# Optimization experiments

Hardware: AMD Instinct MI355X
Metric: run time of the kernel (lower is better)

The kernel has to match this reference:

```python
import jax, jax.numpy as jnp
import numpy as np

B, C, H, W = 64, 3, 32, 32
HID, PRE, VMAX = 128, 32, 256
IN_DIM = C * 5 - 1  # 14


def setup_inputs() -> dict:
    key = jax.random.key(0)
    ks = jax.random.split(key, 9)
    s = 0.05
    return {
        "x": jax.random.uniform(ks[0], (B, C, H, W), dtype=jnp.float32),
        "W_pre": jax.random.normal(ks[1], (PRE, IN_DIM), dtype=jnp.float32) * s,
        "b_pre": jnp.zeros((PRE,), dtype=jnp.float32),
        "W_ih": jax.random.normal(ks[2], (3 * HID, PRE), dtype=jnp.float32) * s,
        "b_ih": jnp.zeros((3 * HID,), dtype=jnp.float32),
        "W_hh": jax.random.normal(ks[3], (3 * HID, HID), dtype=jnp.float32) * s,
        "b_hh": jnp.zeros((3 * HID,), dtype=jnp.float32),
        "W_post": jax.random.normal(ks[4], (VMAX, HID), dtype=jnp.float32) * s,
        "b_post": jnp.zeros((VMAX,), dtype=jnp.float32),
    }


def _img2input(x):
    # x: [b, c, h, w] -> [b, (h-2)*(w-2)*c, 5c-1], matching torch _img2input
    b, c, h, w = x.shape
    xp = jnp.transpose(x, (0, 2, 3, 1))  # [b,h,w,c]
    tl = xp[:, :-2, :-2, :]
    tc = xp[:, :-2, 1:-1, :]
    tr = xp[:, :-2, 2:, :]
    lf = xp[:, 1:-1, :-2, :]
    ct = xp[:, 1:-1, 1:-1, :]
    base = jnp.concatenate([tl, tc, tr, lf], axis=-1)  # [b,h-2,w-2,4c]
    base = jnp.broadcast_to(base[..., None, :], base.shape[:3] + (c, 4 * c))
    # tail[ic, ic1] = center[ic1] if ic1 < ic else -1
    mask = jnp.arange(c - 1)[None, :] < jnp.arange(c)[:, None]  # [c, c-1]
    tail = jnp.where(mask, ct[..., None, :c - 1], -1.0)  # [b,h-2,w-2,c,c-1]
    y = jnp.concatenate([base, tail], axis=-1)  # [b,h-2,w-2,c,5c-1]
    return y.reshape(b, (h - 2) * (w - 2) * c, 5 * c - 1)


def reference(x, W_pre, b_pre, W_ih, b_ih, W_hh, b_hh, W_post, b_post):
    b, c, h, w = x.shape
    inp = _img2input(x)                                   # [b, T, 5c-1]
    pre = jax.nn.sigmoid(inp @ W_pre.T + b_pre)           # [b, T, PRE]
    xg = pre @ W_ih.T + b_ih                              # [b, T, 3*HID]
    xg_t = jnp.transpose(xg, (1, 0, 2))                   # [T, b, 3*HID]

    def step(h_prev, xt):
        hg = h_prev @ W_hh.T + b_hh
        xr, xz, xn = jnp.split(xt, 3, axis=-1)
        hr, hz, hn = jnp.split(hg, 3, axis=-1)
        r = jax.nn.sigmoid(xr + hr)
        z = jax.nn.sigmoid(xz + hz)
        n = jnp.tanh(xn + r * hn)
        h_new = (1.0 - z) * n + z * h_prev
        return h_new, h_new

    h0 = jnp.zeros((b, W_hh.shape[1]), dtype=x.dtype)
    _, hs = jax.lax.scan(step, h0, xg_t)                  # [T, b, HID]
    hs = jnp.transpose(hs, (1, 0, 2))                     # [b, T, HID]
    out = hs @ W_post.T + b_post                          # [b, T, VMAX]
    vmax = W_post.shape[0]
    out = out.reshape(b, h - 2, w - 2, c, vmax)
    out = jnp.transpose(out, (0, 3, 1, 2, 4))             # [b, c, h-2, w-2, vmax]
    out = jnp.pad(out, ((0, 0), (0, 0), (1, 1), (1, 1), (0, 0)))
    return out  # [b, c, h, w, vmax]
```

## Files before the change

### kernel.cpp

```cpp
#include <hip/hip_runtime.h>
#include <cstdint>

#define B_    64
#define T_    2700
#define HID_  128
#define PRE_  32
#define VMAX_ 256
#define NG_   16
#define NB_   4
#define TCH_  27
#define TSZ_  100

typedef _Float16 half2_t __attribute__((ext_vector_type(2)));
typedef _Float16 half4_t __attribute__((ext_vector_type(4)));
typedef _Float16 half8_t __attribute__((ext_vector_type(8)));
typedef float    f32x4_t __attribute__((ext_vector_type(4)));
union H8u { half8_t v; half2_t p[4]; };

#define MFMA32(A, Bv, C) __builtin_amdgcn_mfma_f32_16x16x32_f16((A), (Bv), (C), 0, 0, 0)

#if __has_builtin(__builtin_amdgcn_fdot2)
__device__ __forceinline__ float FDOT2(half2_t a, half2_t b, float c) {
    return __builtin_amdgcn_fdot2(a, b, c, false);
}
#else
__device__ __forceinline__ float FDOT2(half2_t a, half2_t b, float c) {
    return c + (float)a[0] * (float)b[0] + (float)a[1] * (float)b[1];
}
#endif

__device__ __forceinline__ half2_t mk2(float a, float b) {
    half2_t r; r[0] = (_Float16)a; r[1] = (_Float16)b; return r;
}
__device__ __forceinline__ float fast_sigmoid(float x) {
    float t = __builtin_amdgcn_exp2f(-1.4426950408889634f * x);
    return __builtin_amdgcn_rcpf(1.0f + t);
}
__device__ __forceinline__ float fast_tanh(float x) {
    float t = __builtin_amdgcn_exp2f(2.885390081777927f * x);
    return 1.0f - 2.0f * __builtin_amdgcn_rcpf(t + 1.0f);
}
__device__ __forceinline__ float pick_reg(f32x4_t v, int addr, int sel) {
    float t0 = __int_as_float(__builtin_amdgcn_ds_bpermute(addr, __float_as_int(v[0])));
    float t1 = __int_as_float(__builtin_amdgcn_ds_bpermute(addr, __float_as_int(v[1])));
    float t2 = __int_as_float(__builtin_amdgcn_ds_bpermute(addr, __float_as_int(v[2])));
    float t3 = __int_as_float(__builtin_amdgcn_ds_bpermute(addr, __float_as_int(v[3])));
    float a = (sel & 1) ? t1 : t0;
    float b = (sel & 1) ? t3 : t2;
    return (sel & 2) ? b : a;
}

__global__ __launch_bounds__(256) void k_pre(const float* __restrict__ x,
                                             const float* __restrict__ W_pre,
                                             const float* __restrict__ b_pre,
                                             _Float16* __restrict__ pre16) {
    int tid  = blockIdx.x * 256 + threadIdx.x;
    int i    = tid & 31;
    int rest = tid >> 5;
    int c    = rest % 3;
    int r2   = rest / 3;
    int p    = r2 % 900;
    int b    = r2 / 900;
    int r    = p / 30;
    int cc   = p - r * 30;
    const float* xb = x + b * 3072 + r * 32 + cc;
    float f0 = xb[0],    f1  = xb[1024], f2  = xb[2048];
    float f3 = xb[1],    f4  = xb[1025], f5  = xb[2049];
    float f6 = xb[2],    f7  = xb[1026], f8  = xb[2050];
    float f9 = xb[32],   f10 = xb[1056], f11 = xb[2080];
    float ct0 = xb[33],  ct1 = xb[1057];
    float f12 = (c >= 1) ? ct0 : -1.0f;
    float f13 = (c >= 2) ? ct1 : -1.0f;
    const float* w = W_pre + i * 14;
    float d = b_pre[i];
    d += f0*w[0]  + f1*w[1]  + f2*w[2]  + f3*w[3]  + f4*w[4]  + f5*w[5]  + f6*w[6]
       + f7*w[7]  + f8*w[8]  + f9*w[9]  + f10*w[10] + f11*w[11] + f12*w[12] + f13*w[13];

    int t  = p * 3 + c;
    int g  = b >> 2;
    int cs = b & 3;
    size_t base = ((size_t)g * T_ + t) * 128;
    int idx = ((i >> 3) << 5) | (cs << 3) | (i & 7);
    pre16[base + idx] = (_Float16)fast_sigmoid(d);
}

__global__ __launch_bounds__(512) void k_xg(const float* __restrict__ W_ih,
                                            const float* __restrict__ b_ih,
                                            const float* __restrict__ b_hh,
                                            const _Float16* __restrict__ pre16,
                                            _Float16* __restrict__ xg16) {
    const int tid = threadIdx.x;
    const int g   = blockIdx.x / TCH_;
    const int tc  = blockIdx.x % TCH_;
    const int u3  = (tid >> 6) * 16 + ((tid & 63) >> 2);
    const int c4  = tid & 3;

    half2_t wr[16], wz[16], wn[16];
    const float* Wr = W_ih + (size_t)u3 * PRE_;
    const float* Wz = W_ih + (size_t)(128 + u3) * PRE_;
    const float* Wn = W_ih + (size_t)(256 + u3) * PRE_;
#pragma unroll
    for (int k2 = 0; k2 < 16; ++k2) {
        wr[k2] = mk2(Wr[2*k2], Wr[2*k2 + 1]);
        wz[k2] = mk2(Wz[2*k2], Wz[2*k2 + 1]);
        wn[k2] = mk2(Wn[2*k2], Wn[2*k2 + 1]);
    }
    const float br = b_ih[u3] + b_hh[u3];
    const float bz = b_ih[128 + u3] + b_hh[128 + u3];
    const float bn = b_ih[256 + u3];

    const char* preg = (const char*)pre16 + ((size_t)g * T_ + (size_t)tc * TSZ_) * 256 + c4 * 16;
    H8u pc0, pc1, pc2, pc3;
    pc0.v = *(const half8_t*)(preg +   0);
    pc1.v = *(const half8_t*)(preg +  64);
    pc2.v = *(const half8_t*)(preg + 128);
    pc3.v = *(const half8_t*)(preg + 192);

    for (int tt = 0; tt < TSZ_; ++tt) {
        const int ttn = (tt + 1 < TSZ_) ? tt + 1 : tt;
        H8u n0, n1, n2, n3;
        n0.v = *(const half8_t*)(preg + (size_t)ttn * 256 +   0);
        n1.v = *(const half8_t*)(preg + (size_t)ttn * 256 +  64);
        n2.v = *(const half8_t*)(preg + (size_t)ttn * 256 + 128);
        n3.v = *(const half8_t*)(preg + (size_t)ttn * 256 + 192);

        float ar = br, az = bz, an = bn;
#pragma unroll
        for (int j2 = 0; j2 < 4; ++j2) { ar = FDOT2(wr[ 0+j2], pc0.p[j2], ar); az = FDOT2(wz[ 0+j2], pc0.p[j2], az); an = FDOT2(wn[ 0+j2], pc0.p[j2], an); }
#pragma unroll
        for (int j2 = 0; j2 < 4; ++j2) { ar = FDOT2(wr[ 4+j2], pc1.p[j2], ar); az = FDOT2(wz[ 4+j2], pc1.p[j2], az); an = FDOT2(wn[ 4+j2], pc1.p[j2], an); }
#pragma unroll
        for (int j2 = 0; j2 < 4; ++j2) { ar = FDOT2(wr[ 8+j2], pc2.p[j2], ar); az = FDOT2(wz[ 8+j2], pc2.p[j2], az); an = FDOT2(wn[ 8+j2], pc2.p[j2], an); }
#pragma unroll
        for (int j2 = 0; j2 < 4; ++j2) { ar = FDOT2(wr[12+j2], pc3.p[j2], ar); az = FDOT2(wz[12+j2], pc3.p[j2], az); an = FDOT2(wn[12+j2], pc3.p[j2], an); }

        const size_t t = (size_t)tc * TSZ_ + tt;
        half4_t o;
        o[0] = (_Float16)ar; o[1] = (_Float16)az; o[2] = (_Float16)an; o[3] = (_Float16)0.f;
        *(half4_t*)((char*)xg16 + (((size_t)g * T_ + t) * 512 + tid) * 8) = o;
        pc0 = n0; pc1 = n1; pc2 = n2; pc3 = n3;
    }
}

__global__ __launch_bounds__(256) void k_wcvt(const float* __restrict__ W_post,
                                              _Float16* __restrict__ w16) {
    int idx = blockIdx.x * 256 + threadIdx.x;
    w16[idx] = (_Float16)W_post[idx];
}

__global__ __launch_bounds__(512, 1) void k_scan(const float* __restrict__ W_hh,
                                                 const float* __restrict__ b_hh,
                                                 const _Float16* __restrict__ xg16,
                                                 _Float16* __restrict__ hs16) {
    __shared__ __align__(16) _Float16 hbuf[2][4][4][4][8];

    const int tid  = threadIdx.x;
    const int g    = blockIdx.x;
    const int w    = tid >> 6;
    const int lane = tid & 63;
    const int lo   = lane & 15;
    const int hi   = lane >> 4;
    const int c4   = lane & 3;
    const int row  = w * 16 + lo;

    half8_t Ar[4], Az[4], Ahn[4];
#pragma unroll
    for (int kc = 0; kc < 4; ++kc) {
        half8_t ar, az, an;
#pragma unroll
        for (int j = 0; j < 8; ++j) {
            int k = kc * 32 + hi * 8 + j;
            ar[j] = (_Float16)W_hh[row * HID_ + k];
            az[j] = (_Float16)W_hh[(128 + row) * HID_ + k];
            an[j] = (_Float16)W_hh[(256 + row) * HID_ + k];
        }
        Ar[kc] = ar; Az[kc] = az; Ahn[kc] = an;
    }

    const int u3 = w * 16 + (lane >> 2);
    const float bhn = b_hh[256 + u3];
    const int srcaddr = ((((lane >> 4) << 4) | c4) << 2);
    const int sel     = (lane >> 2) & 3;

    const char* xgp = (const char*)xg16 + ((size_t)g * T_ * 512 + tid) * 8;
    _Float16* hsb = hs16 + (size_t)(g * NB_ + c4) * T_ * HID_ + u3;

    const int kc_w = u3 >> 5;
    const int hi_w = (u3 >> 3) & 3;
    const int j_w  = u3 & 7;

    ((uint32_t*)hbuf)[tid] = 0u;

    half4_t xh = *(const half4_t*)(xgp);
    float hprev = 0.0f;
    __syncthreads();

    for (int t = 0; t < T_; ++t) {
        const int tn = (t + 1 < T_) ? (t + 1) : t;
        half4_t xhn = *(const half4_t*)(xgp + (size_t)tn * 4096);

        const int rb = t & 1;
        half8_t hB[4];
#pragma unroll
        for (int kc = 0; kc < 4; ++kc)
            hB[kc] = *(const half8_t*)&hbuf[rb][kc][hi][c4][0];

        const f32x4_t Z4 = {0.f, 0.f, 0.f, 0.f};
        f32x4_t r = Z4, z = Z4, n = Z4;
        r = MFMA32(Ar[0],  hB[0], r);
        z = MFMA32(Az[0],  hB[0], z);
        n = MFMA32(Ahn[0], hB[0], n);
        r = MFMA32(Ar[1],  hB[1], r);
        z = MFMA32(Az[1],  hB[1], z);
        n = MFMA32(Ahn[1], hB[1], n);
        r = MFMA32(Ar[2],  hB[2], r);
        z = MFMA32(Az[2],  hB[2], z);
        n = MFMA32(Ahn[2], hB[2], n);
        r = MFMA32(Ar[3],  hB[3], r);
        z = MFMA32(Az[3],  hB[3], z);
        n = MFMA32(Ahn[3], hB[3], n);

        float srr = pick_reg(r, srcaddr, sel) + (float)xh[0];
        float szz = pick_reg(z, srcaddr, sel) + (float)xh[1];
        float shn = pick_reg(n, srcaddr, sel) + bhn;
        float sxn = (float)xh[2];

        float rg   = fast_sigmoid(srr);
        float zg   = fast_sigmoid(szz);
        float ng   = fast_tanh(sxn + rg * shn);
        float hnew = ng + zg * (hprev - ng);
        hprev = hnew;
        _Float16 h16 = (_Float16)hnew;

        hbuf[rb ^ 1][kc_w][hi_w][c4][j_w] = h16;
        hsb[(size_t)t * HID_] = h16;

        xh = xhn;

        asm volatile("s_waitcnt lgkmcnt(0)" ::: "memory");
        __builtin_amdgcn_s_barrier();
    }
}

__global__ __launch_bounds__(512, 2) void k_post(const _Float16* __restrict__ w16,
                                                 const float* __restrict__ b_post,
                                                 const _Float16* __restrict__ hs,
                                                 float* __restrict__ out) {
    const int tid  = threadIdx.x;
    const int blk  = blockIdx.x;
    const int i    = blk & 31;
    const int rest = blk >> 5;
    const int ch   = rest % 3;
    const int b    = rest / 3;
    float* outb = out + ((size_t)(b * 3 + ch) * 1024 + i * 32) * VMAX_;

    const float4 z4 = {0.f, 0.f, 0.f, 0.f};
    if (i == 0 || i == 31) {
        float4* o4 = (float4*)outb;
#pragma unroll
        for (int k = 0; k < 4; ++k) o4[k * 512 + tid] = z4;
        return;
    }
    if (tid < 64)       ((float4*)outb)[tid] = z4;
    else if (tid < 128) ((float4*)(outb + 31 * VMAX_))[tid - 64] = z4;

    const int wv   = tid >> 6;
    const int lane = tid & 63;
    const int lo   = lane & 15;
    const int hi   = lane >> 4;
    const int t0   = (i - 1) * 90 + ch;
    const _Float16* hsb = hs + (size_t)b * T_ * HID_;

    half8_t Af[2][4], Bf[2][4];
#pragma unroll
    for (int mt = 0; mt < 2; ++mt) {
        int m = mt * 16 + lo; if (m > 29) m = 29;
        const _Float16* ap = hsb + (size_t)(t0 + 3 * m) * HID_ + hi * 8;
#pragma unroll
        for (int kc = 0; kc < 4; ++kc) Af[mt][kc] = *(const half8_t*)(ap + kc * 32);
    }
    const int vb = wv * 32;
#pragma unroll
    for (int nt = 0; nt < 2; ++nt) {
        const _Float16* bp = w16 + (size_t)(vb + nt * 16 + lo) * HID_ + hi * 8;
#pragma unroll
        for (int kc = 0; kc < 4; ++kc) Bf[nt][kc] = *(const half8_t*)(bp + kc * 32);
    }
    const float bp0 = b_post[vb + lo];
    const float bp1 = b_post[vb + 16 + lo];

    f32x4_t a00 = {0.f,0.f,0.f,0.f}, a01 = a00, a10 = a00, a11 = a00;
#pragma unroll
    for (int kc = 0; kc < 4; ++kc) {
        a00 = MFMA32(Af[0][kc], Bf[0][kc], a00);
        a01 = MFMA32(Af[0][kc], Bf[1][kc], a01);
        a10 = MFMA32(Af[1][kc], Bf[0][kc], a10);
        a11 = MFMA32(Af[1][kc], Bf[1][kc], a11);
    }

#pragma unroll
    for (int q = 0; q < 4; ++q) {
        {
            float* orow = outb + (size_t)(1 + 4 * hi + q) * VMAX_;
            orow[vb + lo]      = a00[q] + bp0;
            orow[vb + 16 + lo] = a01[q] + bp1;
        }
        if (4 * hi + q <= 13) {
            float* orow = outb + (size_t)(17 + 4 * hi + q) * VMAX_;
            orow[vb + lo]      = a10[q] + bp0;
            orow[vb + 16 + lo] = a11[q] + bp1;
        }
    }
}

extern "C" void kernel_launch(void* const* d_in, const int* in_sizes, int n_in,
                              void* d_out, int out_size, void* d_ws, size_t ws_size,
                              hipStream_t stream) {
    const float* x      = (const float*)d_in[0];
    const float* W_pre  = (const float*)d_in[1];
    const float* b_pre  = (const float*)d_in[2];
    const float* W_ih   = (const float*)d_in[3];
    const float* b_ih   = (const float*)d_in[4];
    const float* W_hh   = (const float*)d_in[5];
    const float* b_hh   = (const float*)d_in[6];
    const float* W_post = (const float*)d_in[7];
    const float* b_post = (const float*)d_in[8];
    float* out = (float*)d_out;

    const size_t pre_bytes = (size_t)NG_ * T_ * 256;
    const size_t xg_bytes  = (size_t)NG_ * T_ * 512 * 8;
    _Float16* pre16 = (_Float16*)d_ws;
    _Float16* w16   = (_Float16*)d_ws;
    _Float16* xg    = (_Float16*)((char*)d_ws + pre_bytes);
    _Float16* hs16  = (_Float16*)((char*)d_ws + pre_bytes + xg_bytes);

    k_pre <<<21600, 256, 0, stream>>>(x, W_pre, b_pre, pre16);
    k_xg  <<<NG_ * TCH_, 512, 0, stream>>>(W_ih, b_ih, b_hh, pre16, xg);
    k_wcvt<<<128, 256, 0, stream>>>(W_post, w16);
    k_scan<<<NG_, 512, 0, stream>>>(W_hh, b_hh, xg, hs16);
    k_post<<<6144, 512, 0, stream>>>(w16, b_post, hs16, out);
}
```

Before: 1.986 ms.

## Interleave two batch groups per scan block to overlap MFMA with gate math

Each scan block now runs two independent batch groups, and the launch drops from 16 blocks to 8. The steps are software-pipelined so that one group's recurrent MFMA chain is issued while the other group's gate nonlinearities and hidden-state update are computed. The aim is to hide MFMA and LDS latency on the serial recurrence critical path. In exchange each block does twice the work over twice as many barriers, uses half as many CUs, and performs one redundant MFMA set at the final step.

```diff
diff --git a/kernel.cpp b/kernel.cpp
--- a/kernel.cpp
+++ b/kernel.cpp
@@ -8,6 +8,7 @@
 #define VMAX_ 256
 #define NG_   16
 #define NB_   4
+#define NBLK_ 8
 #define TCH_  27
 #define TSZ_  100
 
@@ -155,7 +156,7 @@
     __shared__ __align__(16) _Float16 hbuf[2][4][4][4][8];
 
     const int tid  = threadIdx.x;
-    const int g    = blockIdx.x;
+    const int bg   = blockIdx.x;
     const int w    = tid >> 6;
     const int lane = tid & 63;
     const int lo   = lane & 15;
@@ -182,8 +183,10 @@
     const int srcaddr = ((((lane >> 4) << 4) | c4) << 2);
     const int sel     = (lane >> 2) & 3;
 
-    const char* xgp = (const char*)xg16 + ((size_t)g * T_ * 512 + tid) * 8;
-    _Float16* hsb = hs16 + (size_t)(g * NB_ + c4) * T_ * HID_ + u3;
+    const char* xgpA = (const char*)xg16 + ((size_t)(2 * bg)     * T_ * 512 + tid) * 8;
+    const char* xgpB = (const char*)xg16 + ((size_t)(2 * bg + 1) * T_ * 512 + tid) * 8;
+    _Float16* hsbA = hs16 + (size_t)(8 * bg + c4)     * T_ * HID_ + u3;
+    _Float16* hsbB = hs16 + (size_t)(8 * bg + 4 + c4) * T_ * HID_ + u3;
 
     const int kc_w = u3 >> 5;
     const int hi_w = (u3 >> 3) & 3;
@@ -191,54 +194,91 @@
 
     ((uint32_t*)hbuf)[tid] = 0u;
 
-    half4_t xh = *(const half4_t*)(xgp);
-    float hprev = 0.0f;
+    half4_t xhA = *(const half4_t*)(xgpA);
+    half4_t xhB = *(const half4_t*)(xgpB);
+    float hpA = 0.0f, hpB = 0.0f;
+
+    const f32x4_t Z4 = {0.f, 0.f, 0.f, 0.f};
+    f32x4_t rA = Z4, zA = Z4, nA = Z4;
+    f32x4_t rB = Z4, zB = Z4, nB = Z4;
     __syncthreads();
 
     for (int t = 0; t < T_; ++t) {
         const int tn = (t + 1 < T_) ? (t + 1) : t;
-        half4_t xhn = *(const half4_t*)(xgp + (size_t)tn * 4096);
-
-        const int rb = t & 1;
-        half8_t hB[4];
-#pragma unroll
-        for (int kc = 0; kc < 4; ++kc)
-            hB[kc] = *(const half8_t*)&hbuf[rb][kc][hi][c4][0];
-
-        const f32x4_t Z4 = {0.f, 0.f, 0.f, 0.f};
-        f32x4_t r = Z4, z = Z4, n = Z4;
-        r = MFMA32(Ar[0],  hB[0], r);
-        z = MFMA32(Az[0],  hB[0], z);
-        n = MFMA32(Ahn[0], hB[0], n);
-        r = MFMA32(Ar[1],  hB[1], r);
-        z = MFMA32(Az[1],  hB[1], z);
-        n = MFMA32(Ahn[1], hB[1], n);
-        r = MFMA32(Ar[2],  hB[2], r);
-        z = MFMA32(Az[2],  hB[2], z);
-        n = MFMA32(Ahn[2], hB[2], n);
-        r = MFMA32(Ar[3],  hB[3], r);
-        z = MFMA32(Az[3],  hB[3], z);
-        n = MFMA32(Ahn[3], hB[3], n);
-
-        float srr = pick_reg(r, srcaddr, sel) + (float)xh[0];
-        float szz = pick_reg(z, srcaddr, sel) + (float)xh[1];
-        float shn = pick_reg(n, srcaddr, sel) + bhn;
-        float sxn = (float)xh[2];
-
-        float rg   = fast_sigmoid(srr);
-        float zg   = fast_sigmoid(szz);
-        float ng   = fast_tanh(sxn + rg * shn);
-        float hnew = ng + zg * (hprev - ng);
-        hprev = hnew;
-        _Float16 h16 = (_Float16)hnew;
-
-        hbuf[rb ^ 1][kc_w][hi_w][c4][j_w] = h16;
-        hsb[(size_t)t * HID_] = h16;
-
-        xh = xhn;
-
-        asm volatile("s_waitcnt lgkmcnt(0)" ::: "memory");
-        __builtin_amdgcn_s_barrier();
+        half4_t xAn = *(const half4_t*)(xgpA + (size_t)tn * 4096);
+        half4_t xBn = *(const half4_t*)(xgpB + (size_t)tn * 4096);
+
+        {
+            half8_t b0 = *(const half8_t*)&hbuf[1][0][hi][c4][0];
+            half8_t b1 = *(const half8_t*)&hbuf[1][1][hi][c4][0];
+            half8_t b2 = *(const half8_t*)&hbuf[1][2][hi][c4][0];
+            half8_t b3 = *(const half8_t*)&hbuf[1][3][hi][c4][0];
+            rB = Z4; zB = Z4; nB = Z4;
+            rB = MFMA32(Ar[0],  b0, rB);
+            zB = MFMA32(Az[0],  b0, zB);
+            nB = MFMA32(Ahn[0], b0, nB);
+            rB = MFMA32(Ar[1],  b1, rB);
+            zB = MFMA32(Az[1],  b1, zB);
+            nB = MFMA32(Ahn[1], b1, nB);
+            rB = MFMA32(Ar[2],  b2, rB);
+            zB = MFMA32(Az[2],  b2, zB);
+            nB = MFMA32(Ahn[2], b2, nB);
+            rB = MFMA32(Ar[3],  b3, rB);
+            zB = MFMA32(Az[3],  b3, zB);
+            nB = MFMA32(Ahn[3], b3, nB);
+
+            float srr = pick_reg(rA, srcaddr, sel) + (float)xhA[0];
+            float szz = pick_reg(zA, srcaddr, sel) + (float)xhA[1];
+            float shn = pick_reg(nA, srcaddr, sel) + bhn;
+            float rg   = fast_sigmoid(srr);
+            float zg   = fast_sigmoid(szz);
+            float ng   = fast_tanh((float)xhA[2] + rg * shn);
+            float hnew = ng + zg * (hpA - ng);
+            hpA = hnew;
+            _Float16 h16 = (_Float16)hnew;
+            hbuf[0][kc_w][hi_w][c4][j_w] = h16;
+            hsbA[(size_t)t * HID_] = h16;
+
+            asm volatile("s_waitcnt lgkmcnt(0)" ::: "memory");
+            __builtin_amdgcn_s_barrier();
+        }
+
+        {
+            half8_t a0 = *(const half8_t*)&hbuf[0][0][hi][c4][0];
+            half8_t a1 = *(const half8_t*)&hbuf[0][1][hi][c4][0];
+            half8_t a2 = *(const half8_t*)&hbuf[0][2][hi][c4][0];
+            half8_t a3 = *(const half8_t*)&hbuf[0][3][hi][c4][0];
+            rA = Z4; zA = Z4; nA = Z4;
+            rA = MFMA32(Ar[0],  a0, rA);
+            zA = MFMA32(Az[0],  a0, zA);
+            nA = MFMA32(Ahn[0], a0, nA);
+            rA = MFMA32(Ar[1],  a1, rA);
+            zA = MFMA32(Az[1],  a1, zA);
+            nA = MFMA32(Ahn[1], a1, nA);
+            rA = MFMA32(Ar[2],  a2, rA);
+            zA = MFMA32(Az[2],  a2, zA);
+            nA = MFMA32(Ahn[2], a2, nA);
+            rA = MFMA32(Ar[3],  a3, rA);
+            zA = MFMA32(Az[3],  a3, zA);
+            nA = MFMA32(Ahn[3], a3, nA);
+
+            float srr = pick_reg(rB, srcaddr, sel) + (float)xhB[0];
+            float szz = pick_reg(zB, srcaddr, sel) + (float)xhB[1];
+            float shn = pick_reg(nB, srcaddr, sel) + bhn;
+            float rg   = fast_sigmoid(srr);
+            float zg   = fast_sigmoid(szz);
+            float ng   = fast_tanh((float)xhB[2] + rg * shn);
+            float hnew = ng + zg * (hpB - ng);
+            hpB = hnew;
+            _Float16 h16 = (_Float16)hnew;
+            hbuf[1][kc_w][hi_w][c4][j_w] = h16;
+            hsbB[(size_t)t * HID_] = h16;
+
+            asm volatile("s_waitcnt lgkmcnt(0)" ::: "memory");
+            __builtin_amdgcn_s_barrier();
+        }
+
+        xhA = xAn; xhB = xBn;
     }
 }
 
@@ -337,6 +377,6 @@
     k_pre <<<21600, 256, 0, stream>>>(x, W_pre, b_pre, pre16);
     k_xg  <<<NG_ * TCH_, 512, 0, stream>>>(W_ih, b_ih, b_hh, pre16, xg);
     k_wcvt<<<128, 256, 0, stream>>>(W_post, w16);
-    k_scan<<<NG_, 512, 0, stream>>>(W_hh, b_hh, xg, hs16);
+    k_scan<<<NBLK_, 512, 0, stream>>>(W_hh, b_hh, xg, hs16);
     k_post<<<6144, 512, 0, stream>>>(w16, b_post, hs16, out);
 }
```

Measured after the change: 3.261 ms. +64.2%, slower.

## Pack 16 batch columns per scan block to fill MFMA N dimension

Applied to the files above, without the earlier changes.

The recurrent scan now processes 16 batch sequences per block using the full 16-column MFMA B operand, instead of 4 sequences per block with replicated columns. Each lane reads its four accumulator rows directly and computes four hidden units, removing the bpermute redistribution. The xg buffer layout written by k_xg is reorganized so each scan thread loads its gate inputs contiguously. Fewer blocks run the serial scan, and per-lane ALU work per step increases.

```diff
diff --git a/kernel.cpp b/kernel.cpp
--- a/kernel.cpp
+++ b/kernel.cpp
@@ -8,6 +8,7 @@
 #define VMAX_ 256
 #define NG_   16
 #define NB_   4
+#define NG4_  4
 #define TCH_  27
 #define TSZ_  100
 
@@ -39,15 +40,6 @@
 __device__ __forceinline__ float fast_tanh(float x) {
     float t = __builtin_amdgcn_exp2f(2.885390081777927f * x);
     return 1.0f - 2.0f * __builtin_amdgcn_rcpf(t + 1.0f);
-}
-__device__ __forceinline__ float pick_reg(f32x4_t v, int addr, int sel) {
-    float t0 = __int_as_float(__builtin_amdgcn_ds_bpermute(addr, __float_as_int(v[0])));
-    float t1 = __int_as_float(__builtin_amdgcn_ds_bpermute(addr, __float_as_int(v[1])));
-    float t2 = __int_as_float(__builtin_amdgcn_ds_bpermute(addr, __float_as_int(v[2])));
-    float t3 = __int_as_float(__builtin_amdgcn_ds_bpermute(addr, __float_as_int(v[3])));
-    float a = (sel & 1) ? t1 : t0;
-    float b = (sel & 1) ? t3 : t2;
-    return (sel & 2) ? b : a;
 }
 
 __global__ __launch_bounds__(256) void k_pre(const float* __restrict__ x,
@@ -109,6 +101,15 @@
     const float bz = b_ih[128 + u3] + b_hh[128 + u3];
     const float bn = b_ih[256 + u3];
 
+    const int bb   = g * 4 + c4;
+    const int g4   = bb >> 4;
+    const int col  = bb & 15;
+    const int w_   = u3 >> 4;
+    const int rw   = u3 & 15;
+    const int tid2 = w_ * 64 + (rw >> 2) * 16 + col;
+    const int qo   = (rw & 3) * 8;
+    char* outp = (char*)xg16 + ((size_t)g4 * T_ * 512 + tid2) * 32 + qo;
+
     const char* preg = (const char*)pre16 + ((size_t)g * T_ + (size_t)tc * TSZ_) * 256 + c4 * 16;
     H8u pc0, pc1, pc2, pc3;
     pc0.v = *(const half8_t*)(preg +   0);
@@ -137,7 +138,7 @@
         const size_t t = (size_t)tc * TSZ_ + tt;
         half4_t o;
         o[0] = (_Float16)ar; o[1] = (_Float16)az; o[2] = (_Float16)an; o[3] = (_Float16)0.f;
-        *(half4_t*)((char*)xg16 + (((size_t)g * T_ + t) * 512 + tid) * 8) = o;
+        *(half4_t*)(outp + t * 16384) = o;
         pc0 = n0; pc1 = n1; pc2 = n2; pc3 = n3;
     }
 }
@@ -152,15 +153,14 @@
                                                  const float* __restrict__ b_hh,
                                                  const _Float16* __restrict__ xg16,
                                                  _Float16* __restrict__ hs16) {
-    __shared__ __align__(16) _Float16 hbuf[2][4][4][4][8];
+    __shared__ __align__(16) _Float16 hbuf[2][4][4][16][8];
 
     const int tid  = threadIdx.x;
-    const int g    = blockIdx.x;
+    const int g4   = blockIdx.x;
     const int w    = tid >> 6;
     const int lane = tid & 63;
     const int lo   = lane & 15;
     const int hi   = lane >> 4;
-    const int c4   = lane & 3;
     const int row  = w * 16 + lo;
 
     half8_t Ar[4], Az[4], Ahn[4];
@@ -177,65 +177,66 @@
         Ar[kc] = ar; Az[kc] = az; Ahn[kc] = an;
     }
 
-    const int u3 = w * 16 + (lane >> 2);
-    const float bhn = b_hh[256 + u3];
-    const int srcaddr = ((((lane >> 4) << 4) | c4) << 2);
-    const int sel     = (lane >> 2) & 3;
-
-    const char* xgp = (const char*)xg16 + ((size_t)g * T_ * 512 + tid) * 8;
-    _Float16* hsb = hs16 + (size_t)(g * NB_ + c4) * T_ * HID_ + u3;
-
-    const int kc_w = u3 >> 5;
-    const int hi_w = (u3 >> 3) & 3;
-    const int j_w  = u3 & 7;
-
-    ((uint32_t*)hbuf)[tid] = 0u;
-
-    half4_t xh = *(const half4_t*)(xgp);
-    float hprev = 0.0f;
+    const int u0 = w * 16 + 4 * hi;
+    const f32x4_t bhn4 = *(const f32x4_t*)(b_hh + 256 + u0);
+
+    const char* xgp = (const char*)xg16 + ((size_t)g4 * T_ * 512 + tid) * 32;
+    _Float16* hsb = hs16 + (size_t)(g4 * 16 + lo) * T_ * HID_ + u0;
+
+    const int kc_w = w >> 1;
+    const int hi_w = (2 * w + (hi >> 1)) & 3;
+    const int j_w  = 4 * (hi & 1);
+
+#pragma unroll
+    for (int zz = 0; zz < 4; ++zz) ((uint32_t*)hbuf)[zz * 512 + tid] = 0u;
+
+    half8_t x0 = *(const half8_t*)(xgp);
+    half8_t x1 = *(const half8_t*)(xgp + 16);
+    f32x4_t hp = {0.f, 0.f, 0.f, 0.f};
     __syncthreads();
 
     for (int t = 0; t < T_; ++t) {
-        const int tn = (t + 1 < T_) ? (t + 1) : t;
-        half4_t xhn = *(const half4_t*)(xgp + (size_t)tn * 4096);
+        const size_t on = (size_t)((t + 1 < T_) ? t + 1 : t) * 16384;
+        half8_t x0n = *(const half8_t*)(xgp + on);
+        half8_t x1n = *(const half8_t*)(xgp + on + 16);
 
         const int rb = t & 1;
-        half8_t hB[4];
-#pragma unroll
-        for (int kc = 0; kc < 4; ++kc)
-            hB[kc] = *(const half8_t*)&hbuf[rb][kc][hi][c4][0];
+        half8_t hB0 = *(const half8_t*)&hbuf[rb][0][hi][lo][0];
+        half8_t hB1 = *(const half8_t*)&hbuf[rb][1][hi][lo][0];
+        half8_t hB2 = *(const half8_t*)&hbuf[rb][2][hi][lo][0];
+        half8_t hB3 = *(const half8_t*)&hbuf[rb][3][hi][lo][0];
 
         const f32x4_t Z4 = {0.f, 0.f, 0.f, 0.f};
         f32x4_t r = Z4, z = Z4, n = Z4;
-        r = MFMA32(Ar[0],  hB[0], r);
-        z = MFMA32(Az[0],  hB[0], z);
-        n = MFMA32(Ahn[0], hB[0], n);
-        r = MFMA32(Ar[1],  hB[1], r);
-        z = MFMA32(Az[1],  hB[1], z);
-        n = MFMA32(Ahn[1], hB[1], n);
-        r = MFMA32(Ar[2],  hB[2], r);
-        z = MFMA32(Az[2],  hB[2], z);
-        n = MFMA32(Ahn[2], hB[2], n);
-        r = MFMA32(Ar[3],  hB[3], r);
-        z = MFMA32(Az[3],  hB[3], z);
-        n = MFMA32(Ahn[3], hB[3], n);
-
-        float srr = pick_reg(r, srcaddr, sel) + (float)xh[0];
-        float szz = pick_reg(z, srcaddr, sel) + (float)xh[1];
-        float shn = pick_reg(n, srcaddr, sel) + bhn;
-        float sxn = (float)xh[2];
-
-        float rg   = fast_sigmoid(srr);
-        float zg   = fast_sigmoid(szz);
-        float ng   = fast_tanh(sxn + rg * shn);
-        float hnew = ng + zg * (hprev - ng);
-        hprev = hnew;
-        _Float16 h16 = (_Float16)hnew;
-
-        hbuf[rb ^ 1][kc_w][hi_w][c4][j_w] = h16;
-        hsb[(size_t)t * HID_] = h16;
-
-        xh = xhn;
+        r = MFMA32(Ar[0],  hB0, r);
+        z = MFMA32(Az[0],  hB0, z);
+        n = MFMA32(Ahn[0], hB0, n);
+        r = MFMA32(Ar[1],  hB1, r);
+        z = MFMA32(Az[1],  hB1, z);
+        n = MFMA32(Ahn[1], hB1, n);
+        r = MFMA32(Ar[2],  hB2, r);
+        z = MFMA32(Az[2],  hB2, z);
+        n = MFMA32(Ahn[2], hB2, n);
+        r = MFMA32(Ar[3],  hB3, r);
+        z = MFMA32(Az[3],  hB3, z);
+        n = MFMA32(Ahn[3], hB3, n);
+
+        half4_t hq;
+#pragma unroll
+        for (int q = 0; q < 4; ++q) {
+            half8_t xv = (q < 2) ? x0 : x1;
+            const int o = (q & 1) * 4;
+            float rg = fast_sigmoid(r[q] + (float)xv[o]);
+            float zg = fast_sigmoid(z[q] + (float)xv[o + 1]);
+            float ng = fast_tanh((float)xv[o + 2] + rg * (n[q] + bhn4[q]));
+            float hv = ng + zg * (hp[q] - ng);
+            hp[q] = hv;
+            hq[q] = (_Float16)hv;
+        }
+        *(half4_t*)&hbuf[rb ^ 1][kc_w][hi_w][lo][j_w] = hq;
+        *(half4_t*)(hsb + (size_t)t * HID_) = hq;
+
+        x0 = x0n; x1 = x1n;
 
         asm volatile("s_waitcnt lgkmcnt(0)" ::: "memory");
         __builtin_amdgcn_s_barrier();
@@ -328,7 +329,7 @@
     float* out = (float*)d_out;
 
     const size_t pre_bytes = (size_t)NG_ * T_ * 256;
-    const size_t xg_bytes  = (size_t)NG_ * T_ * 512 * 8;
+    const size_t xg_bytes  = (size_t)NG4_ * T_ * 512 * 32;
     _Float16* pre16 = (_Float16*)d_ws;
     _Float16* w16   = (_Float16*)d_ws;
     _Float16* xg    = (_Float16*)((char*)d_ws + pre_bytes);
@@ -337,6 +338,6 @@
     k_pre <<<21600, 256, 0, stream>>>(x, W_pre, b_pre, pre16);
     k_xg  <<<NG_ * TCH_, 512, 0, stream>>>(W_ih, b_ih, b_hh, pre16, xg);
     k_wcvt<<<128, 256, 0, stream>>>(W_post, w16);
-    k_scan<<<NG_, 512, 0, stream>>>(W_hh, b_hh, xg, hs16);
+    k_scan<<<NG4_, 512, 0, stream>>>(W_hh, b_hh, xg, hs16);
     k_post<<<6144, 512, 0, stream>>>(w16, b_post, hs16, out);
 }
```

Measured after the change: 2.051 ms. 3.3% more time.
